# Optimization experiments

Hardware: AMD Instinct MI355X
Metric: run time of the kernel (lower is better)

The kernel has to match this reference:

```python
import jax, jax.numpy as jnp
import numpy as np

AUDIO_DIM, SEM_DIM, ATTN_DIM = 512, 768, 128


def setup_inputs() -> dict:
    key = jax.random.key(0)
    ks = jax.random.split(key, 12)
    B, T, T_sem = 8, 4096, 1024
    s = lambda d: 1.0 / np.sqrt(d)
    return {
        "x_ct": jax.random.normal(ks[0], (B, AUDIO_DIM, T), jnp.float32),
        "sem_btd": jax.random.normal(ks[1], (B, T_sem, SEM_DIM), jnp.float32),
        "ln_w": jnp.ones((AUDIO_DIM,), jnp.float32),
        "ln_b": jnp.zeros((AUDIO_DIM,), jnp.float32),
        "Wq": jax.random.normal(ks[2], (AUDIO_DIM, ATTN_DIM), jnp.float32) * s(AUDIO_DIM),
        "bq": jnp.zeros((ATTN_DIM,), jnp.float32),
        "Wk": jax.random.normal(ks[3], (SEM_DIM, ATTN_DIM), jnp.float32) * s(SEM_DIM),
        "bk": jnp.zeros((ATTN_DIM,), jnp.float32),
        "Wv": jax.random.normal(ks[4], (SEM_DIM, ATTN_DIM), jnp.float32) * s(SEM_DIM),
        "bv": jnp.zeros((ATTN_DIM,), jnp.float32),
        "Wo": jax.random.normal(ks[5], (ATTN_DIM, AUDIO_DIM), jnp.float32) * s(ATTN_DIM),
        "bo": jnp.zeros((AUDIO_DIM,), jnp.float32),
    }


def _layernorm(x, w, b, eps=1e-5):
    mu = jnp.mean(x, axis=-1, keepdims=True)
    var = jnp.mean(jnp.square(x - mu), axis=-1, keepdims=True)
    return (x - mu) * jax.lax.rsqrt(var + eps) * w + b


def reference(x_ct, sem_btd, ln_w, ln_b, Wq, bq, Wk, bk, Wv, bv, Wo, bo):
    # x_ct: [B, C, T] -> [B, T, C]
    x = jnp.swapaxes(x_ct, 1, 2)
    x = _layernorm(x, ln_w, ln_b)
    Q = x @ Wq + bq                      # [B, T, A]
    K = sem_btd @ Wk + bk                # [B, S, A]
    V = sem_btd @ Wv + bv                # [B, S, A]
    scale = ATTN_DIM ** -0.5
    attn = jnp.einsum("bta,bsa->bts", Q, K) * scale
    attn = jax.nn.softmax(attn, axis=-1)  # dropout: eval mode (identity)
    ctx = jnp.einsum("bts,bsa->bta", attn, V)
    delta = ctx @ Wo + bo                # [B, T, C]
    return jnp.swapaxes(delta, 1, 2)     # [B, C, T]
```

## Files before the change

kernel.cpp:

```cpp
#include <hip/hip_runtime.h>
#include <hip/hip_bf16.h>
#include <math.h>

#define BATCH 8
#define TDIM 4096
#define SDIM 1024
#define CDIM 512
#define DDIM 768
#define ADIM 128

typedef short s8v __attribute__((ext_vector_type(8)));
typedef float f4v __attribute__((ext_vector_type(4)));

__device__ __forceinline__ short f2bf(float f) {
    unsigned u = __float_as_uint(f);
    u += 0x7fffu + ((u >> 16) & 1u);
    return (short)(u >> 16);
}
__device__ __forceinline__ float bf2f(short s) {
    return __uint_as_float(((unsigned)(unsigned short)s) << 16);
}
__device__ __forceinline__ f4v mfma16(s8v a, s8v b, f4v c) {
    return __builtin_amdgcn_mfma_f32_16x16x32_bf16(a, b, c, 0, 0, 0);
}
__device__ __forceinline__ void gl_lds16(const short* g, short* l) {
    __builtin_amdgcn_global_load_lds(
        (const __attribute__((address_space(1))) unsigned int*)g,
        (__attribute__((address_space(3))) unsigned int*)l, 16, 0, 0);
}

__global__ __launch_bounds__(256) void prep(
    const float* __restrict__ Wq, const float* __restrict__ Wk,
    const float* __restrict__ Wv, const float* __restrict__ Wo,
    const float* __restrict__ lnw, const float* __restrict__ lnb,
    short* __restrict__ WqT, short* __restrict__ WkT,
    short* __restrict__ WvT, short* __restrict__ WoT,
    float* __restrict__ uq, float* __restrict__ vq)
{
    __shared__ float r1[128], r2[128];
    if (blockIdx.x < 256) {
        int gid = blockIdx.x * 256 + threadIdx.x;
        {
            int k = gid >> 7, n = gid & 127;
            int idx = (k >> 6) * 8192 + n * 64 + ((((k >> 3) & 7) ^ (n & 7)) * 8) + (k & 7);
            WqT[idx] = f2bf(Wq[gid] * lnw[k]);
        }
        #pragma unroll
        for (int i = 0; i < 2; ++i) {
            int e = gid + i * 65536;
            if (e < 98304) {
                int k = e >> 7, n = e & 127;
                WkT[n * 768 + k] = f2bf(Wk[e]);
                WvT[n * 768 + k] = f2bf(Wv[e]);
            }
        }
        {
            int k = gid >> 9, c = gid & 511;
            WoT[c * 128 + k] = f2bf(Wo[gid]);
        }
    } else {
        const int a = threadIdx.x & 127, h = threadIdx.x >> 7;
        const int c = (blockIdx.x - 256) * 2 + h;
        float wv = Wq[c * 128 + a];
        float s1 = bf2f(f2bf(lnw[c] * wv));
        float s2 = lnb[c] * wv;
        if (h) { r1[a] = s1; r2[a] = s2; }
        __syncthreads();
        if (!h) {
            atomicAdd(&uq[a], s1 + r1[a]);
            atomicAdd(&vq[a], s2 + r2[a]);
        }
    }
}

__global__ __launch_bounds__(512, 4) void mid(
    const float* __restrict__ x, const short* __restrict__ WqI,
    const float* __restrict__ uq, const float* __restrict__ vq,
    const float* __restrict__ bq, short* __restrict__ Qb,
    const float* __restrict__ sem,
    const short* __restrict__ WkT, const float* __restrict__ bk,
    const short* __restrict__ WvT, const float* __restrict__ bv,
    short* __restrict__ Kb, short* __restrict__ Vb)
{
    __shared__ __align__(16) char smem[55296];
    const int tid = threadIdx.x, lane = tid & 63, wave = tid >> 6;
    const int ln15 = lane & 15, q = lane >> 4, kq = q * 8;
    const int bid = blockIdx.x;

    if ((bid % 3) != 2) {
        const int ln_id = (bid / 3) * 2 + (bid % 3);
        short* sXp = (short*)smem;
        short* sWp = (short*)(smem + 18432);
        float* redwp = (float*)(smem + 51200);
        const int b = ln_id >> 6;
        const int t0 = (ln_id & 63) * 64;
        const float* xb = x + (size_t)b * CDIM * TDIM + t0;

        const int rg = lane >> 4;
        const int g  = rg & 1;
        const int L  = lane & 15;
        const int t4 = L * 4;
        const int crow = wave * 4 + rg;

        float ps1[4] = {0.f,0.f,0.f,0.f}, ps2[4] = {0.f,0.f,0.f,0.f};
        const int wr = wave & 3, wc = wave >> 2;
        const int m = wr * 16 + ln15;
        const int swzm = (m >> 2) & 7;
        f4v acc[4];
        #pragma unroll
        for (int j = 0; j < 4; ++j) acc[j] = (f4v)0.0f;

        float4 xv[2];

#define PROC_X(BUF) do {                                                      \
    _Pragma("unroll")                                                         \
    for (int i = 0; i < 2; ++i) {                                             \
        float4 v = xv[i];                                                     \
        ps1[0] += v.x; ps2[0] += v.x * v.x;                                   \
        ps1[1] += v.y; ps2[1] += v.y * v.y;                                   \
        ps1[2] += v.z; ps2[2] += v.z * v.z;                                   \
        ps1[3] += v.w; ps2[3] += v.w * v.w;                                   \
        float o0 = __shfl_xor(v.x, 16); float o1 = __shfl_xor(v.y, 16);       \
        float o2 = __shfl_xor(v.z, 16); float o3 = __shfl_xor(v.w, 16);       \
        const int c   = crow + i * 32;                                        \
        const int cdw = c & ~1;                                               \
        unsigned wA, wB; int tA, tB;                                          \
        if (g == 0) {                                                         \
            tA = t4; tB = t4 + 1;                                             \
            wA = (unsigned short)f2bf(v.x) | ((unsigned)(unsigned short)f2bf(o0) << 16); \
            wB = (unsigned short)f2bf(v.y) | ((unsigned)(unsigned short)f2bf(o1) << 16); \
        } else {                                                              \
            tA = t4 + 2; tB = t4 + 3;                                         \
            wA = (unsigned short)f2bf(o2) | ((unsigned)(unsigned short)f2bf(v.z) << 16); \
            wB = (unsigned short)f2bf(o3) | ((unsigned)(unsigned short)f2bf(v.w) << 16); \
        }                                                                     \
        *(unsigned*)&sXp[(BUF) * 4608 + tA * 72 + (((cdw >> 3) ^ ((tA >> 2) & 7)) * 8) + (cdw & 7)] = wA; \
        *(unsigned*)&sXp[(BUF) * 4608 + tB * 72 + (((cdw >> 3) ^ ((tB >> 2) & 7)) * 8) + (cdw & 7)] = wB; \
    }                                                                         \
} while (0)

        xv[0] = *(const float4*)&xb[(size_t)crow * TDIM + t4];
        xv[1] = *(const float4*)&xb[(size_t)(crow + 32) * TDIM + t4];
        #pragma unroll
        for (int i = 0; i < 2; ++i) {
            int gi = i * 512 + wave * 64;
            gl_lds16(&WqI[(size_t)(gi + lane) * 8], &sWp[gi * 8]);
        }
        PROC_X(0);
        __syncthreads();

        for (int kc = 0; kc < 8; ++kc) {
            const int cur = kc & 1;
            if (kc < 7) {
                const float* xc = xb + (size_t)(kc + 1) * 64 * TDIM;
                xv[0] = *(const float4*)&xc[(size_t)crow * TDIM + t4];
                xv[1] = *(const float4*)&xc[(size_t)(crow + 32) * TDIM + t4];
                const short* wch = WqI + (size_t)(kc + 1) * 8192;
                #pragma unroll
                for (int i = 0; i < 2; ++i) {
                    int gi = i * 512 + wave * 64;
                    gl_lds16(&wch[(size_t)(gi + lane) * 8], &sWp[(cur ^ 1) * 8192 + gi * 8]);
                }
            }
            #pragma unroll
            for (int kk = 0; kk < 2; ++kk) {
                s8v a = *(const s8v*)&sXp[cur * 4608 + m * 72 + (((kk * 4 + q) ^ swzm) * 8)];
                #pragma unroll
                for (int j = 0; j < 4; ++j) {
                    int n = wc * 64 + j * 16 + ln15;
                    s8v bb = *(const s8v*)&sWp[cur * 8192 + n * 64 + (((kk * 4 + q) ^ (n & 7)) * 8)];
                    acc[j] = mfma16(a, bb, acc[j]);
                }
            }
            if (kc < 7) PROC_X(cur ^ 1);
            __syncthreads();
        }
#undef PROC_X

        #pragma unroll
        for (int mk = 16; mk <= 32; mk <<= 1) {
            #pragma unroll
            for (int jj = 0; jj < 4; ++jj) {
                ps1[jj] += __shfl_xor(ps1[jj], mk);
                ps2[jj] += __shfl_xor(ps2[jj], mk);
            }
        }
        if (lane < 16) {
            #pragma unroll
            for (int jj = 0; jj < 4; ++jj) {
                redwp[((wave * 16 + L) * 4 + jj) * 2 + 0] = ps1[jj];
                redwp[((wave * 16 + L) * 4 + jj) * 2 + 1] = ps2[jj];
            }
        }
        __syncthreads();

        float u4[4], v4[4];
        #pragma unroll
        for (int j = 0; j < 4; ++j) {
            int col = wc * 64 + j * 16 + ln15;
            u4[j] = uq[col]; v4[j] = vq[col] + bq[col];
        }
        const float scale = 0.08838834764831845f;
        const int quad = wr * 4 + q;
        #pragma unroll
        for (int r = 0; r < 4; ++r) {
            float s1 = 0.f, s2 = 0.f;
            #pragma unroll
            for (int w = 0; w < 8; ++w) {
                float2 p = *(const float2*)&redwp[((w * 16 + quad) * 4 + r) * 2];
                s1 += p.x; s2 += p.y;
            }
            float mu = s1 * (1.f / 512.f);
            float var = s2 * (1.f / 512.f) - mu * mu;
            float rs = rsqrtf(var + 1e-5f);
            int t = t0 + wr * 16 + q * 4 + r;
            #pragma unroll
            for (int j = 0; j < 4; ++j) {
                float qv = (rs * (acc[j][r] - mu * u4[j]) + v4[j]) * scale;
                Qb[((size_t)b * TDIM + t) * ADIM + (wc * 64 + j * 16 + ln15)] = f2bf(qv);
            }
        }
    } else {
        const int kv_id = bid / 3;
        if (tid < 256) {
            short* sA  = (short*)smem;
            short* sWk = (short*)(smem + 2560);
            const int r0 = kv_id * 32;
            const int b = r0 >> 10, sbase = r0 & 1023;
            const int kv = wave >> 1;
            const int mh = wave & 1;
            const int m  = mh * 16 + ln15;

            f4v acc[8];
            #pragma unroll
            for (int j = 0; j < 8; ++j) acc[j] = (f4v)0.0f;

            const int srow = tid >> 3;
            const int sk4  = (tid & 7) * 4;

            for (int kc = 0; kc < DDIM / 32; ++kc) {
                __syncthreads();
                {
                    float4 f = *(const float4*)&sem[(size_t)(r0 + srow) * DDIM + kc * 32 + sk4];
                    uint2 pk;
                    pk.x = (unsigned short)f2bf(f.x) | ((unsigned)(unsigned short)f2bf(f.y) << 16);
                    pk.y = (unsigned short)f2bf(f.z) | ((unsigned)(unsigned short)f2bf(f.w) << 16);
                    *(uint2*)&sA[srow * 40 + sk4] = pk;
                }
                #pragma unroll
                for (int i = 0; i < 2; ++i) {
                    int idx8 = i * 256 + tid;
                    int n = idx8 >> 2, k8 = (idx8 & 3) * 8;
                    *(s8v*)&sWk[n * 40 + k8] = *(const s8v*)&WkT[(size_t)n * 768 + kc * 32 + k8];
                    *(s8v*)&sWk[5120 + n * 40 + k8] = *(const s8v*)&WvT[(size_t)n * 768 + kc * 32 + k8];
                }
                __syncthreads();
                s8v a = *(const s8v*)&sA[m * 40 + kq];
                #pragma unroll
                for (int j = 0; j < 8; ++j) {
                    s8v bb = *(const s8v*)&sWk[kv * 5120 + (j * 16 + ln15) * 40 + kq];
                    acc[j] = mfma16(a, bb, acc[j]);
                }
            }
            const int s_in_b = sbase + mh * 16 + q * 4;
            if (kv == 0) {
                #pragma unroll
                for (int j = 0; j < 8; ++j) {
                    int col = j * 16 + ln15;
                    float bias = bk[col];
                    #pragma unroll
                    for (int r = 0; r < 4; ++r)
                        Kb[((size_t)b * SDIM + s_in_b + r) * ADIM + col] = f2bf(acc[j][r] + bias);
                }
            } else {
                #pragma unroll
                for (int j = 0; j < 8; ++j) {
                    int col = j * 16 + ln15;
                    float bias = bv[col];
                    uint2 pk;
                    pk.x = (unsigned short)f2bf(acc[j][0] + bias) | ((unsigned)(unsigned short)f2bf(acc[j][1] + bias) << 16);
                    pk.y = (unsigned short)f2bf(acc[j][2] + bias) | ((unsigned)(unsigned short)f2bf(acc[j][3] + bias) << 16);
                    *(uint2*)&Vb[((size_t)b * ADIM + col) * SDIM + s_in_b] = pk;
                }
            }
        } else {
            for (int kc = 0; kc < DDIM / 32; ++kc) { __syncthreads(); __syncthreads(); }
        }
    }
}

__global__ __launch_bounds__(256) void attn(
    const short* __restrict__ Qb, const short* __restrict__ Kb,
    const short* __restrict__ Vb, short* __restrict__ Cx)
{
    __shared__ __align__(16) short sK [2][64 * 128];
    __shared__ __align__(16) short sVT[2][128 * 64];
    __shared__ __align__(16) short sP [64 * 64];
    const int tid = threadIdx.x, lane = tid & 63, wave = tid >> 6;
    const int ln15 = lane & 15, q = lane >> 4, kq = q * 8;
    const int b = blockIdx.x >> 6;
    const int t0 = (blockIdx.x & 63) * 64;
    const int m = wave * 16 + ln15;

    const int krow = tid >> 4, kkb = tid & 15;
    const int varow = tid >> 3, vkb = tid & 7;

    s8v qf[4];
    {
        const short* qp = Qb + ((size_t)b * TDIM + t0 + m) * ADIM + kq;
        #pragma unroll
        for (int kc = 0; kc < 4; ++kc) qf[kc] = *(const s8v*)(qp + kc * 32);
    }
    s8v ones;
    #pragma unroll
    for (int j = 0; j < 8; ++j) ones[j] = (short)0x3F80;

    f4v accO[8]; f4v accL = (f4v)0.0f;
    #pragma unroll
    for (int j = 0; j < 8; ++j) accO[j] = (f4v)0.0f;

    const short* Kbase = Kb + (size_t)b * SDIM * ADIM;
    const short* Vbase = Vb + (size_t)b * ADIM * SDIM;
    s8v rk[4], rv[4];

    #pragma unroll
    for (int i = 0; i < 4; ++i) {
        rk[i] = *(const s8v*)(Kbase + (size_t)(i * 16 + krow) * ADIM + kkb * 8);
        rv[i] = *(const s8v*)(Vbase + (size_t)(i * 32 + varow) * SDIM + vkb * 8);
    }
    #pragma unroll
    for (int i = 0; i < 4; ++i) {
        int r = i * 16 + krow;
        *(s8v*)&sK[0][r * 128 + ((kkb ^ (r & 15)) * 8)] = rk[i];
        int a = i * 32 + varow;
        *(s8v*)&sVT[0][a * 64 + ((vkb ^ (a & 7)) * 8)] = rv[i];
    }
    __syncthreads();

    for (int sc = 0; sc < SDIM / 64; ++sc) {
        const int cur = sc & 1;
        if (sc < 15) {
            const int s0n = (sc + 1) * 64;
            #pragma unroll
            for (int i = 0; i < 4; ++i) {
                rk[i] = *(const s8v*)(Kbase + (size_t)(s0n + i * 16 + krow) * ADIM + kkb * 8);
                rv[i] = *(const s8v*)(Vbase + (size_t)(i * 32 + varow) * SDIM + s0n + vkb * 8);
            }
        }
        #pragma unroll
        for (int j = 0; j < 4; ++j) {
            f4v sacc = (f4v)0.0f;
            const int row = j * 16 + ln15;
            #pragma unroll
            for (int kc = 0; kc < 4; ++kc) {
                s8v bb = *(const s8v*)&sK[cur][row * 128 + (((kc * 4 + q) ^ (row & 15)) * 8)];
                sacc = mfma16(qf[kc], bb, sacc);
            }
            #pragma unroll
            for (int r = 0; r < 4; ++r) {
                float ev = __expf(sacc[r]);
                int prow = wave * 16 + q * 4 + r;
                int pcol = j * 16 + ln15;
                sP[prow * 64 + (((pcol >> 3) ^ (prow & 7)) * 8) + (pcol & 7)] = f2bf(ev);
            }
        }
        #pragma unroll
        for (int kc = 0; kc < 2; ++kc) {
            s8v pa = *(const s8v*)&sP[m * 64 + (((kc * 4 + q) ^ (m & 7)) * 8)];
            accL = mfma16(pa, ones, accL);
            #pragma unroll
            for (int j = 0; j < 8; ++j) {
                int a = j * 16 + ln15;
                s8v bb = *(const s8v*)&sVT[cur][a * 64 + (((kc * 4 + q) ^ (a & 7)) * 8)];
                accO[j] = mfma16(pa, bb, accO[j]);
            }
        }
        if (sc < 15) {
            #pragma unroll
            for (int i = 0; i < 4; ++i) {
                int r = i * 16 + krow;
                *(s8v*)&sK[cur ^ 1][r * 128 + ((kkb ^ (r & 15)) * 8)] = rk[i];
                int a = i * 32 + varow;
                *(s8v*)&sVT[cur ^ 1][a * 64 + ((vkb ^ (a & 7)) * 8)] = rv[i];
            }
        }
        __syncthreads();
    }
    #pragma unroll
    for (int r = 0; r < 4; ++r) {
        float rinv = 1.0f / accL[r];
        int t = t0 + wave * 16 + q * 4 + r;
        #pragma unroll
        for (int j = 0; j < 8; ++j) {
            int col = j * 16 + ln15;
            Cx[((size_t)b * TDIM + t) * ADIM + col] = f2bf(accO[j][r] * rinv);
        }
    }
}

__global__ __launch_bounds__(256) void out_proj(
    const short* __restrict__ Cx, const short* __restrict__ WoT,
    const float* __restrict__ bo, float* __restrict__ out)
{
    __shared__ __align__(16) short sCtx[64 * 136];
    __shared__ __align__(16) char  buf[128 * 136 * 2];
    short* sWoT = (short*)buf;
    float* outT = (float*)buf;
    const int tid = threadIdx.x, lane = tid & 63, wave = tid >> 6;
    const int ln15 = lane & 15, q = lane >> 4, kq = q * 8;
    const int b = blockIdx.x >> 8;
    const int rem = blockIdx.x & 255;
    const int t0 = (rem & 63) * 64;
    const int c0 = (rem >> 6) * 128;

    #pragma unroll
    for (int i = 0; i < 4; ++i) {
        int idx8 = i * 256 + tid;
        int row = idx8 >> 4, a8 = (idx8 & 15) * 8;
        *(s8v*)&sCtx[row * 136 + a8] = *(const s8v*)&Cx[((size_t)b * TDIM + t0 + row) * ADIM + a8];
    }
    #pragma unroll
    for (int i = 0; i < 8; ++i) {
        int idx8 = i * 256 + tid;
        int n = idx8 >> 4, k8 = (idx8 & 15) * 8;
        *(s8v*)&sWoT[n * 136 + k8] = *(const s8v*)&WoT[(size_t)(c0 + n) * ADIM + k8];
    }
    __syncthreads();
    f4v acc[8];
    #pragma unroll
    for (int j = 0; j < 8; ++j) acc[j] = (f4v)0.0f;
    const int m = wave * 16 + ln15;
    #pragma unroll
    for (int kc = 0; kc < 4; ++kc) {
        s8v a = *(const s8v*)&sCtx[m * 136 + kc * 32 + kq];
        #pragma unroll
        for (int j = 0; j < 8; ++j) {
            s8v bb = *(const s8v*)&sWoT[(j * 16 + ln15) * 136 + kc * 32 + kq];
            acc[j] = mfma16(a, bb, acc[j]);
        }
    }
    __syncthreads();
    #pragma unroll
    for (int j = 0; j < 8; ++j) {
        int cl = j * 16 + ln15;
        float bias = bo[c0 + cl];
        #pragma unroll
        for (int r = 0; r < 4; ++r) {
            int tl = wave * 16 + q * 4 + r;
            outT[cl * 68 + tl] = acc[j][r] + bias;
        }
    }
    __syncthreads();
    #pragma unroll
    for (int i = 0; i < 8; ++i) {
        int idx4 = i * 256 + tid;
        int c = idx4 >> 4, t4 = (idx4 & 15) * 4;
        float4 v = *(const float4*)&outT[c * 68 + t4];
        *(float4*)&out[((size_t)b * CDIM + c0 + c) * TDIM + t0 + t4] = v;
    }
}

extern "C" void kernel_launch(void* const* d_in, const int* in_sizes, int n_in,
                              void* d_out, int out_size, void* d_ws, size_t ws_size,
                              hipStream_t stream) {
    const float* x   = (const float*)d_in[0];
    const float* sem = (const float*)d_in[1];
    const float* lnw = (const float*)d_in[2];
    const float* lnb = (const float*)d_in[3];
    const float* Wq  = (const float*)d_in[4];
    const float* bq  = (const float*)d_in[5];
    const float* Wk  = (const float*)d_in[6];
    const float* bk  = (const float*)d_in[7];
    const float* Wv  = (const float*)d_in[8];
    const float* bv  = (const float*)d_in[9];
    const float* Wo  = (const float*)d_in[10];
    const float* bo  = (const float*)d_in[11];
    float* out = (float*)d_out;

    short* ws  = (short*)d_ws;
    short* Qb  = ws;
    short* Kb  = Qb  + (size_t)BATCH * TDIM * ADIM;
    short* Vb  = Kb  + (size_t)BATCH * SDIM * ADIM;
    short* Cx  = Vb  + (size_t)BATCH * SDIM * ADIM;
    short* WqT = Cx  + (size_t)BATCH * TDIM * ADIM;
    short* WkT = WqT + 128 * 512;
    short* WvT = WkT + 128 * 768;
    short* WoT = WvT + 128 * 768;
    float* uq  = (float*)(WoT + 512 * 128);
    float* vq  = uq + 128;

    hipMemsetAsync(uq, 0, 256 * sizeof(float), stream);
    hipLaunchKernelGGL(prep, dim3(512), dim3(256), 0, stream,
                       Wq, Wk, Wv, Wo, lnw, lnb, WqT, WkT, WvT, WoT, uq, vq);
    hipLaunchKernelGGL(mid,  dim3(768), dim3(512), 0, stream,
                       x, WqT, uq, vq, bq, Qb, sem, WkT, bk, WvT, bv, Kb, Vb);
    hipLaunchKernelGGL(attn, dim3(512), dim3(256), 0, stream, Qb, Kb, Vb, Cx);
    hipLaunchKernelGGL(out_proj, dim3(2048), dim3(256), 0, stream, Cx, WoT, bo, out);
}
```

Before: 232.9 us.

## Double query rows per attention block, use exp2, restructure out_proj with register weights

The attention kernel now handles 128 query rows per block (two 64-row halves) so each K/V tile staged in shared memory is reused twice. This halves the grid to 256 blocks and raises register pressure. Q is pre-scaled by log2(e)/sqrt(A) so softmax can use exp2f instead of __expf. The output projection keeps Wo fragments in registers and loops over 8 time chunks per block. It writes float4 results straight to the transposed output, dropping the LDS transpose staging and cutting the grid to 512 blocks.

Result: slower. 249.7 us (+7.2%).

```diff
diff --git a/kernel.cpp b/kernel.cpp
--- a/kernel.cpp
+++ b/kernel.cpp
@@ -200,7 +200,7 @@
             int col = wc * 64 + j * 16 + ln15;
             u4[j] = uq[col]; v4[j] = vq[col] + bq[col];
         }
-        const float scale = 0.08838834764831845f;
+        const float scale = 0.12751744f;
         const int quad = wr * 4 + q;
         #pragma unroll
         for (int r = 0; r < 4; ++r) {
@@ -295,29 +295,34 @@
 {
     __shared__ __align__(16) short sK [2][64 * 128];
     __shared__ __align__(16) short sVT[2][128 * 64];
-    __shared__ __align__(16) short sP [64 * 64];
+    __shared__ __align__(16) short sP [128 * 64];
     const int tid = threadIdx.x, lane = tid & 63, wave = tid >> 6;
     const int ln15 = lane & 15, q = lane >> 4, kq = q * 8;
-    const int b = blockIdx.x >> 6;
-    const int t0 = (blockIdx.x & 63) * 64;
+    const int b = blockIdx.x >> 5;
+    const int t0 = (blockIdx.x & 31) * 128;
     const int m = wave * 16 + ln15;
 
     const int krow = tid >> 4, kkb = tid & 15;
     const int varow = tid >> 3, vkb = tid & 7;
 
-    s8v qf[4];
+    s8v qf0[4], qf1[4];
     {
-        const short* qp = Qb + ((size_t)b * TDIM + t0 + m) * ADIM + kq;
-        #pragma unroll
-        for (int kc = 0; kc < 4; ++kc) qf[kc] = *(const s8v*)(qp + kc * 32);
+        const short* qp0 = Qb + ((size_t)b * TDIM + t0 + m) * ADIM + kq;
+        const short* qp1 = qp0 + (size_t)64 * ADIM;
+        #pragma unroll
+        for (int kc = 0; kc < 4; ++kc) {
+            qf0[kc] = *(const s8v*)(qp0 + kc * 32);
+            qf1[kc] = *(const s8v*)(qp1 + kc * 32);
+        }
     }
     s8v ones;
     #pragma unroll
     for (int j = 0; j < 8; ++j) ones[j] = (short)0x3F80;
 
-    f4v accO[8]; f4v accL = (f4v)0.0f;
+    f4v accO0[8], accO1[8];
+    f4v accL0 = (f4v)0.0f, accL1 = (f4v)0.0f;
     #pragma unroll
-    for (int j = 0; j < 8; ++j) accO[j] = (f4v)0.0f;
+    for (int j = 0; j < 8; ++j) { accO0[j] = (f4v)0.0f; accO1[j] = (f4v)0.0f; }
 
     const short* Kbase = Kb + (size_t)b * SDIM * ADIM;
     const short* Vbase = Vb + (size_t)b * ADIM * SDIM;
@@ -349,30 +354,35 @@
         }
         #pragma unroll
         for (int j = 0; j < 4; ++j) {
-            f4v sacc = (f4v)0.0f;
+            f4v s0 = (f4v)0.0f, s1 = (f4v)0.0f;
             const int row = j * 16 + ln15;
             #pragma unroll
             for (int kc = 0; kc < 4; ++kc) {
                 s8v bb = *(const s8v*)&sK[cur][row * 128 + (((kc * 4 + q) ^ (row & 15)) * 8)];
-                sacc = mfma16(qf[kc], bb, sacc);
+                s0 = mfma16(qf0[kc], bb, s0);
+                s1 = mfma16(qf1[kc], bb, s1);
             }
             #pragma unroll
             for (int r = 0; r < 4; ++r) {
-                float ev = __expf(sacc[r]);
                 int prow = wave * 16 + q * 4 + r;
                 int pcol = j * 16 + ln15;
-                sP[prow * 64 + (((pcol >> 3) ^ (prow & 7)) * 8) + (pcol & 7)] = f2bf(ev);
+                int slot = (((pcol >> 3) ^ (prow & 7)) * 8) + (pcol & 7);
+                sP[prow * 64 + slot] = f2bf(exp2f(s0[r]));
+                sP[(prow + 64) * 64 + slot] = f2bf(exp2f(s1[r]));
             }
         }
         #pragma unroll
         for (int kc = 0; kc < 2; ++kc) {
-            s8v pa = *(const s8v*)&sP[m * 64 + (((kc * 4 + q) ^ (m & 7)) * 8)];
-            accL = mfma16(pa, ones, accL);
+            s8v pa0 = *(const s8v*)&sP[m * 64 + (((kc * 4 + q) ^ (m & 7)) * 8)];
+            s8v pa1 = *(const s8v*)&sP[(m + 64) * 64 + (((kc * 4 + q) ^ (m & 7)) * 8)];
+            accL0 = mfma16(pa0, ones, accL0);
+            accL1 = mfma16(pa1, ones, accL1);
             #pragma unroll
             for (int j = 0; j < 8; ++j) {
                 int a = j * 16 + ln15;
                 s8v bb = *(const s8v*)&sVT[cur][a * 64 + (((kc * 4 + q) ^ (a & 7)) * 8)];
-                accO[j] = mfma16(pa, bb, accO[j]);
+                accO0[j] = mfma16(pa0, bb, accO0[j]);
+                accO1[j] = mfma16(pa1, bb, accO1[j]);
             }
         }
         if (sc < 15) {
@@ -388,12 +398,14 @@
     }
     #pragma unroll
     for (int r = 0; r < 4; ++r) {
-        float rinv = 1.0f / accL[r];
+        float rinv0 = 1.0f / accL0[r];
+        float rinv1 = 1.0f / accL1[r];
         int t = t0 + wave * 16 + q * 4 + r;
         #pragma unroll
         for (int j = 0; j < 8; ++j) {
             int col = j * 16 + ln15;
-            Cx[((size_t)b * TDIM + t) * ADIM + col] = f2bf(accO[j][r] * rinv);
+            Cx[((size_t)b * TDIM + t) * ADIM + col] = f2bf(accO0[j][r] * rinv0);
+            Cx[((size_t)b * TDIM + t + 64) * ADIM + col] = f2bf(accO1[j][r] * rinv1);
         }
     }
 }
@@ -402,61 +414,54 @@
     const short* __restrict__ Cx, const short* __restrict__ WoT,
     const float* __restrict__ bo, float* __restrict__ out)
 {
-    __shared__ __align__(16) short sCtx[64 * 136];
-    __shared__ __align__(16) char  buf[128 * 136 * 2];
-    short* sWoT = (short*)buf;
-    float* outT = (float*)buf;
+    __shared__ __align__(16) short sCtx[64 * 128];
     const int tid = threadIdx.x, lane = tid & 63, wave = tid >> 6;
     const int ln15 = lane & 15, q = lane >> 4, kq = q * 8;
-    const int b = blockIdx.x >> 8;
-    const int rem = blockIdx.x & 255;
-    const int t0 = (rem & 63) * 64;
-    const int c0 = (rem >> 6) * 128;
-
+    const int cc = blockIdx.x & 7;
+    const int tt = (blockIdx.x >> 3) & 7;
+    const int b  = blockIdx.x >> 6;
+    const int c0 = cc * 64;
+    const int t0 = tt * 512;
+    const int m = wave * 16 + ln15;
+
+    s8v wf[4][4];
+    float bias[4];
     #pragma unroll
-    for (int i = 0; i < 4; ++i) {
-        int idx8 = i * 256 + tid;
-        int row = idx8 >> 4, a8 = (idx8 & 15) * 8;
-        *(s8v*)&sCtx[row * 136 + a8] = *(const s8v*)&Cx[((size_t)b * TDIM + t0 + row) * ADIM + a8];
-    }
-    #pragma unroll
-    for (int i = 0; i < 8; ++i) {
-        int idx8 = i * 256 + tid;
-        int n = idx8 >> 4, k8 = (idx8 & 15) * 8;
-        *(s8v*)&sWoT[n * 136 + k8] = *(const s8v*)&WoT[(size_t)(c0 + n) * ADIM + k8];
-    }
-    __syncthreads();
-    f4v acc[8];
-    #pragma unroll
-    for (int j = 0; j < 8; ++j) acc[j] = (f4v)0.0f;
-    const int m = wave * 16 + ln15;
-    #pragma unroll
-    for (int kc = 0; kc < 4; ++kc) {
-        s8v a = *(const s8v*)&sCtx[m * 136 + kc * 32 + kq];
-        #pragma unroll
-        for (int j = 0; j < 8; ++j) {
-            s8v bb = *(const s8v*)&sWoT[(j * 16 + ln15) * 136 + kc * 32 + kq];
-            acc[j] = mfma16(a, bb, acc[j]);
-        }
-    }
-    __syncthreads();
-    #pragma unroll
-    for (int j = 0; j < 8; ++j) {
-        int cl = j * 16 + ln15;
-        float bias = bo[c0 + cl];
-        #pragma unroll
-        for (int r = 0; r < 4; ++r) {
-            int tl = wave * 16 + q * 4 + r;
-            outT[cl * 68 + tl] = acc[j][r] + bias;
-        }
-    }
-    __syncthreads();
-    #pragma unroll
-    for (int i = 0; i < 8; ++i) {
-        int idx4 = i * 256 + tid;
-        int c = idx4 >> 4, t4 = (idx4 & 15) * 4;
-        float4 v = *(const float4*)&outT[c * 68 + t4];
-        *(float4*)&out[((size_t)b * CDIM + c0 + c) * TDIM + t0 + t4] = v;
+    for (int j = 0; j < 4; ++j) {
+        #pragma unroll
+        for (int kc = 0; kc < 4; ++kc)
+            wf[j][kc] = *(const s8v*)&WoT[(size_t)(c0 + j * 16 + ln15) * 128 + kc * 32 + kq];
+        bias[j] = bo[c0 + j * 16 + ln15];
+    }
+
+    const int krow = tid >> 4, kkb = tid & 15;
+    const short* cxb = Cx + ((size_t)b * TDIM + t0) * ADIM;
+    float* outb = out + (size_t)b * CDIM * TDIM;
+
+    for (int tc = 0; tc < 8; ++tc) {
+        __syncthreads();
+        #pragma unroll
+        for (int i = 0; i < 4; ++i) {
+            int r = i * 16 + krow;
+            *(s8v*)&sCtx[r * 128 + ((kkb ^ (r & 15)) * 8)] =
+                *(const s8v*)&cxb[(size_t)(tc * 64 + r) * ADIM + kkb * 8];
+        }
+        __syncthreads();
+        s8v a[4];
+        #pragma unroll
+        for (int kc = 0; kc < 4; ++kc)
+            a[kc] = *(const s8v*)&sCtx[m * 128 + (((kc * 4 + q) ^ (m & 15)) * 8)];
+        #pragma unroll
+        for (int j = 0; j < 4; ++j) {
+            f4v acc = (f4v)0.0f;
+            #pragma unroll
+            for (int kc = 0; kc < 4; ++kc)
+                acc = mfma16(a[kc], wf[j][kc], acc);
+            float4 o = { acc[0] + bias[j], acc[1] + bias[j],
+                         acc[2] + bias[j], acc[3] + bias[j] };
+            *(float4*)&outb[(size_t)(c0 + j * 16 + ln15) * TDIM
+                            + t0 + tc * 64 + wave * 16 + q * 4] = o;
+        }
     }
 }
 
@@ -494,6 +499,6 @@
                        Wq, Wk, Wv, Wo, lnw, lnb, WqT, WkT, WvT, WoT, uq, vq);
     hipLaunchKernelGGL(mid,  dim3(768), dim3(512), 0, stream,
                        x, WqT, uq, vq, bq, Qb, sem, WkT, bk, WvT, bv, Kb, Vb);
-    hipLaunchKernelGGL(attn, dim3(512), dim3(256), 0, stream, Qb, Kb, Vb, Cx);
-    hipLaunchKernelGGL(out_proj, dim3(2048), dim3(256), 0, stream, Cx, WoT, bo, out);
-}
+    hipLaunchKernelGGL(attn, dim3(256), dim3(256), 0, stream, Qb, Kb, Vb, Cx);
+    hipLaunchKernelGGL(out_proj, dim3(512), dim3(256), 0, stream, Cx, WoT, bo, out);
+}
```
